# Optimization experiments

Hardware: AMD Instinct MI355X
Metric: run time of the kernel (lower is better)

Reference implementation:

```python
import jax, jax.numpy as jnp
import numpy as np

EMBED_DIM = 1024
NUM_HEADS = 16
HEAD_DIM = EMBED_DIM // NUM_HEADS
B, S = 4, 4096


def maxpool1d_2(x):
    # MaxPooling1D(pool_size=2, strides=2, padding='same'); seq len is even so no padding needed.
    n, l, d = x.shape
    return jnp.max(x.reshape(n, l // 2, 2, d), axis=2)


def setup_inputs() -> dict:
    key = jax.random.key(0)
    ks = jax.random.split(key, 5)
    scale = 1.0 / np.sqrt(EMBED_DIM)
    return {
        "x": jax.random.normal(ks[0], (B, S, EMBED_DIM), dtype=jnp.float32),
        "Wq": jax.random.normal(ks[1], (EMBED_DIM, EMBED_DIM), dtype=jnp.float32) * scale,
        "bq": jnp.zeros((EMBED_DIM,), dtype=jnp.float32),
        "Wk": jax.random.normal(ks[2], (EMBED_DIM, EMBED_DIM), dtype=jnp.float32) * scale,
        "bk": jnp.zeros((EMBED_DIM,), dtype=jnp.float32),
        "Wv": jax.random.normal(ks[3], (EMBED_DIM, EMBED_DIM), dtype=jnp.float32) * scale,
        "bv": jnp.zeros((EMBED_DIM,), dtype=jnp.float32),
        "Wo": jax.random.normal(ks[4], (EMBED_DIM, EMBED_DIM), dtype=jnp.float32) * scale,
        "bo": jnp.zeros((EMBED_DIM,), dtype=jnp.float32),
    }


def _separate_heads_pool(x, batch_size):
    # [B, S, E] -> [B, S, H, hd] -> [B, H, S, hd] -> [B*H, S, hd] -> pooled [B*H, S/2, hd]
    n, s, _ = x.shape
    x = x.reshape(batch_size, s, NUM_HEADS, HEAD_DIM).transpose(0, 2, 1, 3)
    x = x.reshape(batch_size * NUM_HEADS, s, HEAD_DIM)
    return maxpool1d_2(x)


def reference(x, Wq, bq, Wk, bk, Wv, bv, Wo, bo):
    batch_size = x.shape[0]
    q = x @ Wq + bq
    k = x @ Wk + bk
    v = x @ Wv + bv
    q = _separate_heads_pool(q, batch_size)  # [B*H, S/2, hd]
    k = _separate_heads_pool(k, batch_size)
    v = _separate_heads_pool(v, batch_size)
    score = jnp.einsum('nqd,nkd->nqk', q, k) / jnp.sqrt(jnp.float32(HEAD_DIM))
    weights = jax.nn.softmax(score, axis=-1)
    attn = jnp.einsum('nqk,nkd->nqd', weights, v)  # [B*H, S/2, hd]
    attn = maxpool1d_2(attn)  # [B*H, S/4, hd]
    # reshape back: (batch, -1, head_dim*num_heads). NOTE: original reshapes
    # [B*H, S/4, hd] directly to (B, -1, E) without transposing heads back,
    # so we replicate that exact layout.
    attn = attn.reshape(batch_size, -1, HEAD_DIM * NUM_HEADS)  # [B, S/4 (head-major mix), E]
    return attn @ Wo + bo
```

## Files before the change

kernel.cpp:

```cpp
#include <hip/hip_runtime.h>
#include <stdint.h>

typedef __attribute__((ext_vector_type(8))) __bf16 bf16x8;
typedef __attribute__((ext_vector_type(4))) float f32x4;
typedef __attribute__((ext_vector_type(8))) int i32x8;

#define DEV __device__ __forceinline__

DEV unsigned short f2bf(float f) {
  union { float f; uint32_t u; } v; v.f = f;
  return (unsigned short)((v.u + 0x7fffu + ((v.u >> 16) & 1u)) >> 16);
}

DEV uint32_t pk2bf(float lo, float hi) {
  union { float f; uint32_t u; } a, b;
  a.f = lo; b.f = hi;
  return __builtin_amdgcn_perm(b.u + 0x8000u, a.u + 0x8000u, 0x07060302u);
}

DEV void gld16(const void* g, void* l) {
  __builtin_amdgcn_global_load_lds(
      (const __attribute__((address_space(1))) uint32_t*)g,
      (__attribute__((address_space(3))) uint32_t*)l, 16, 0, 0);
}

union Frag8 { i32x8 v; uint4 q[2]; };

__global__ __launch_bounds__(256) void k_cvt_x(const float* __restrict__ x,
                                               uint8_t* __restrict__ x8) {
  size_t t = (size_t)blockIdx.x * 256 + threadIdx.x;
  const float4* xv = (const float4*)x;
  float4 a = xv[t * 2], b = xv[t * 2 + 1];
  int lo = 0, hi = 0;
  lo = __builtin_amdgcn_cvt_pk_fp8_f32(a.x, a.y, lo, false);
  lo = __builtin_amdgcn_cvt_pk_fp8_f32(a.z, a.w, lo, true);
  hi = __builtin_amdgcn_cvt_pk_fp8_f32(b.x, b.y, hi, false);
  hi = __builtin_amdgcn_cvt_pk_fp8_f32(b.z, b.w, hi, true);
  int2 pk; pk.x = lo; pk.y = hi;
  *(int2*)&x8[t * 8] = pk;
}

__global__ void k_cvt_w(const float* __restrict__ W0, const float* __restrict__ W1,
                        const float* __restrict__ W2, const float* __restrict__ W3,
                        uint8_t* __restrict__ W8, unsigned short* __restrict__ WoT) {
  const int z = blockIdx.z;
  const float* W = (z == 0) ? W0 : (z == 1) ? W1 : (z == 2) ? W2 : W3;
  __shared__ float tile[32][33];
  const int n0 = blockIdx.x * 32, k0 = blockIdx.y * 32;
  const int tx = threadIdx.x, ty = threadIdx.y;
  const int tid = ty * 32 + tx;
#pragma unroll
  for (int i = 0; i < 4; i++)
    tile[ty * 4 + i][tx] = W[(size_t)(k0 + ty * 4 + i) * 1024 + n0 + tx];
  __syncthreads();
  if (z < 3) {
    int nn = tid >> 3, kg = tid & 7;
    int w_ = 0;
    w_ = __builtin_amdgcn_cvt_pk_fp8_f32(32.f * tile[kg * 4 + 0][nn],
                                         32.f * tile[kg * 4 + 1][nn], w_, false);
    w_ = __builtin_amdgcn_cvt_pk_fp8_f32(32.f * tile[kg * 4 + 2][nn],
                                         32.f * tile[kg * 4 + 3][nn], w_, true);
    *(uint32_t*)&W8[(size_t)z * 1048576 + (size_t)(n0 + nn) * 1024 + k0 + kg * 4] =
        (uint32_t)w_;
  } else {
#pragma unroll
    for (int i = 0; i < 4; i++)
      WoT[(size_t)(n0 + ty * 4 + i) * 1024 + k0 + tx] = f2bf(tile[tx][ty * 4 + i]);
  }
}

__global__ __launch_bounds__(256) void k_gemm_qkv(
    const uint8_t* __restrict__ A, const uint8_t* __restrict__ W8,
    const float* __restrict__ bq, const float* __restrict__ bk,
    const float* __restrict__ bv,
    unsigned short* __restrict__ Qp, unsigned short* __restrict__ Kp,
    unsigned short* __restrict__ Vt) {
  const int tid = threadIdx.x;
  const int n0 = blockIdx.x * 128, m0 = blockIdx.y * 128;
  const int z = blockIdx.z;
  const uint8_t* Bt = W8 + (size_t)z * 1048576;
  const float* bias = (z == 0) ? bq : (z == 1) ? bk : bv;

  __shared__ __align__(16) uint8_t lA[128 * 128];
  __shared__ __align__(16) uint8_t lB[128 * 128];

  const int lane = tid & 63, w = tid >> 6;
  const int wr = w >> 1, wc = w & 1;
  const int r = lane & 15, qd = lane >> 4;
  const int rl = lane >> 3, sg = lane & 7;

  f32x4 acc[4][4];
#pragma unroll
  for (int i = 0; i < 4; i++)
#pragma unroll
    for (int j = 0; j < 4; j++) acc[i][j] = (f32x4){0.f, 0.f, 0.f, 0.f};

  for (int k0 = 0; k0 < 1024; k0 += 128) {
    __syncthreads();
#pragma unroll
    for (int p = 0; p < 4; p++) {
      int row = (p * 4 + w) * 8 + rl;
      int g = sg ^ (row & 7);
      gld16(&A[(size_t)(m0 + row) * 1024 + k0 + g * 16], &lA[row * 128 + sg * 16]);
      gld16(&Bt[(size_t)(n0 + row) * 1024 + k0 + g * 16], &lB[row * 128 + sg * 16]);
    }
    __syncthreads();
    Frag8 bfr[4];
#pragma unroll
    for (int nt = 0; nt < 4; nt++) {
      int row = wc * 64 + nt * 16 + r;
      int g0 = (2 * qd) ^ (row & 7), g1 = (2 * qd + 1) ^ (row & 7);
      bfr[nt].q[0] = *(const uint4*)&lB[row * 128 + g0 * 16];
      bfr[nt].q[1] = *(const uint4*)&lB[row * 128 + g1 * 16];
    }
#pragma unroll
    for (int mt = 0; mt < 4; mt++) {
      int row = wr * 64 + mt * 16 + r;
      int g0 = (2 * qd) ^ (row & 7), g1 = (2 * qd + 1) ^ (row & 7);
      Frag8 af;
      af.q[0] = *(const uint4*)&lA[row * 128 + g0 * 16];
      af.q[1] = *(const uint4*)&lA[row * 128 + g1 * 16];
#pragma unroll
      for (int nt = 0; nt < 4; nt++)
        acc[mt][nt] = __builtin_amdgcn_mfma_scale_f32_16x16x128_f8f6f4(
            af.v, bfr[nt].v, acc[mt][nt], 0, 0, 0, 0x7f7f7f7f, 0, 0x7f7f7f7f);
    }
  }

  unsigned short* OP = (z == 0) ? Qp : Kp;
#pragma unroll
  for (int nt = 0; nt < 4; nt++) {
    int n = n0 + wc * 64 + nt * 16 + r;
    float bv_ = bias[n];
    int h = n >> 6, d = n & 63;
#pragma unroll
    for (int mt = 0; mt < 4; mt++) {
      int mg = m0 + wr * 64 + mt * 16 + qd * 4;
      int b = mg >> 12, s2 = (mg & 4095) >> 1;
      int bh = b * 16 + h;
      f32x4 a = acc[mt][nt];
      float v0 = fmaxf(a.x, a.y) * 0.03125f + bv_;
      float v1 = fmaxf(a.z, a.w) * 0.03125f + bv_;
      if (z == 2) {
        uint32_t pk = (uint32_t)f2bf(v0) | ((uint32_t)f2bf(v1) << 16);
        *(uint32_t*)&Vt[((size_t)bh * 64 + d) * 2048 + s2] = pk;
      } else {
        size_t base = ((size_t)bh * 2048 + s2) * 64 + d;
        OP[base] = f2bf(v0);
        OP[base + 64] = f2bf(v1);
      }
    }
  }
}

__global__ __launch_bounds__(256) void k_gemm_out(
    const unsigned short* __restrict__ A, const unsigned short* __restrict__ Bt,
    const float* __restrict__ bias, float* __restrict__ fout) {
  const int tid = threadIdx.x;
  const int n0 = blockIdx.x * 128, m0 = blockIdx.y * 128;

  __shared__ __align__(16) unsigned short lA[128 * 64];
  __shared__ __align__(16) unsigned short lB[128 * 64];

  const int lane = tid & 63, w = tid >> 6;
  const int wr = w >> 1, wc = w & 1;
  const int r = lane & 15, qd = lane >> 4;
  const int srow = tid >> 3, sg = tid & 7;

  f32x4 acc[4][4];
#pragma unroll
  for (int i = 0; i < 4; i++)
#pragma unroll
    for (int j = 0; j < 4; j++) acc[i][j] = (f32x4){0.f, 0.f, 0.f, 0.f};

  for (int k0 = 0; k0 < 1024; k0 += 64) {
    __syncthreads();
#pragma unroll
    for (int p = 0; p < 4; p++) {
      int row = p * 32 + srow;
      int gs = sg ^ (row & 7);
      gld16(&A[(size_t)(m0 + row) * 1024 + k0 + gs * 8], &lA[row * 64 + sg * 8]);
      gld16(&Bt[(size_t)(n0 + row) * 1024 + k0 + gs * 8], &lB[row * 64 + sg * 8]);
    }
    __syncthreads();
#pragma unroll
    for (int kf = 0; kf < 2; kf++) {
      bf16x8 af[4], bfr[4];
#pragma unroll
      for (int mt = 0; mt < 4; mt++) {
        int row = wr * 64 + mt * 16 + r;
        int lg = (kf * 4 + qd) ^ (row & 7);
        af[mt] = *(const bf16x8*)&lA[row * 64 + lg * 8];
      }
#pragma unroll
      for (int nt = 0; nt < 4; nt++) {
        int row = wc * 64 + nt * 16 + r;
        int lg = (kf * 4 + qd) ^ (row & 7);
        bfr[nt] = *(const bf16x8*)&lB[row * 64 + lg * 8];
      }
#pragma unroll
      for (int mt = 0; mt < 4; mt++)
#pragma unroll
        for (int nt = 0; nt < 4; nt++)
          acc[mt][nt] = __builtin_amdgcn_mfma_f32_16x16x32_bf16(af[mt], bfr[nt],
                                                               acc[mt][nt], 0, 0, 0);
    }
  }

#pragma unroll
  for (int nt = 0; nt < 4; nt++) {
    int n = n0 + wc * 64 + nt * 16 + r;
    float bv = bias[n];
#pragma unroll
    for (int mt = 0; mt < 4; mt++) {
      int mg = m0 + wr * 64 + mt * 16 + qd * 4;
      f32x4 a = acc[mt][nt];
      fout[(size_t)(mg + 0) * 1024 + n] = a.x + bv;
      fout[(size_t)(mg + 1) * 1024 + n] = a.y + bv;
      fout[(size_t)(mg + 2) * 1024 + n] = a.z + bv;
      fout[(size_t)(mg + 3) * 1024 + n] = a.w + bv;
    }
  }
}

__global__ __launch_bounds__(256) void k_attn(const unsigned short* __restrict__ Qp,
                                              const unsigned short* __restrict__ Kp,
                                              const unsigned short* __restrict__ Vt,
                                              unsigned short* __restrict__ Am) {
  const int tid = threadIdx.x;
  const int qt = blockIdx.x, bh = blockIdx.y;
  const int w = tid >> 6, lane = tid & 63;
  const int r = lane & 15, qd = lane >> 4;
  const int srow = tid >> 3, sg = tid & 7;

  __shared__ __align__(16) unsigned short lK[64 * 64];
  __shared__ __align__(16) unsigned short lV[64 * 64];
  __shared__ __align__(16) unsigned short lP[4][16 * 80];

  const int q0 = qt * 64;
  const int qrow = q0 + w * 16 + r;
  const size_t qbase = ((size_t)bh * 2048 + qrow) * 64;
  const bf16x8 bq0 = *(const bf16x8*)&Qp[qbase + qd * 8];
  const bf16x8 bq1 = *(const bf16x8*)&Qp[qbase + 32 + qd * 8];

  const unsigned short* Kg = Kp + (size_t)bh * 2048 * 64;
  const unsigned short* Vg = Vt + (size_t)bh * 64 * 2048;

  const float K2 = 0.125f * 1.44269504f;

  float lsum = 0.f;
  f32x4 accO[4];
#pragma unroll
  for (int i = 0; i < 4; i++) accO[i] = (f32x4){0.f, 0.f, 0.f, 0.f};

  char* lPw = (char*)&lP[w][0];

  for (int kb = 0; kb < 2048; kb += 64) {
    __syncthreads();
#pragma unroll
    for (int c = 0; c < 2; c++) {
      int row = c * 32 + srow;
      int gs = sg ^ (row & 7);
      gld16(&Kg[(size_t)(kb + row) * 64 + gs * 8], &lK[row * 64 + sg * 8]);
      gld16(&Vg[(size_t)row * 2048 + kb + gs * 8], &lV[row * 64 + sg * 8]);
    }
    __syncthreads();

    f32x4 s[4];
#pragma unroll
    for (int mt = 0; mt < 4; mt++) {
      int row = mt * 16 + r;
      int lg0 = qd ^ (row & 7), lg1 = (4 + qd) ^ (row & 7);
      bf16x8 ak0 = *(const bf16x8*)&lK[row * 64 + lg0 * 8];
      bf16x8 ak1 = *(const bf16x8*)&lK[row * 64 + lg1 * 8];
      s[mt] = (f32x4){0.f, 0.f, 0.f, 0.f};
      s[mt] = __builtin_amdgcn_mfma_f32_16x16x32_bf16(ak0, bq0, s[mt], 0, 0, 0);
      s[mt] = __builtin_amdgcn_mfma_f32_16x16x32_bf16(ak1, bq1, s[mt], 0, 0, 0);
    }

#pragma unroll
    for (int mt = 0; mt < 4; mt++) {
      float p0 = __builtin_amdgcn_exp2f(fmaf(s[mt][0], K2, -0.5f));
      float p1 = __builtin_amdgcn_exp2f(fmaf(s[mt][1], K2, -0.5f));
      float p2 = __builtin_amdgcn_exp2f(fmaf(s[mt][2], K2, -0.5f));
      float p3 = __builtin_amdgcn_exp2f(fmaf(s[mt][3], K2, -0.5f));
      lsum += (p0 + p1) + (p2 + p3);
      uint2 dw; dw.x = pk2bf(p0, p1); dw.y = pk2bf(p2, p3);
      int off = r * 160 + (((2 * mt + (qd >> 1)) ^ (r & 7)) << 4) + ((qd & 1) << 3);
      *(uint2*)(lPw + off) = dw;
    }

    bf16x8 ap0 = *(const bf16x8*)(lPw + r * 160 + ((qd ^ (r & 7)) << 4));
    bf16x8 ap1 = *(const bf16x8*)(lPw + r * 160 + (((4 + qd) ^ (r & 7)) << 4));

#pragma unroll
    for (int nt = 0; nt < 4; nt++) {
      int row = nt * 16 + r;
      int lg0 = qd ^ (row & 7), lg1 = (4 + qd) ^ (row & 7);
      bf16x8 bv0 = *(const bf16x8*)&lV[row * 64 + lg0 * 8];
      bf16x8 bv1 = *(const bf16x8*)&lV[row * 64 + lg1 * 8];
      accO[nt] = __builtin_amdgcn_mfma_f32_16x16x32_bf16(ap0, bv0, accO[nt], 0, 0, 0);
      accO[nt] = __builtin_amdgcn_mfma_f32_16x16x32_bf16(ap1, bv1, accO[nt], 0, 0, 0);
    }
  }

  lsum += __shfl_xor(lsum, 16, 64);
  lsum += __shfl_xor(lsum, 32, 64);
  float linv = 1.f / lsum;
  float inv[4];
#pragma unroll
  for (int g = 0; g < 4; g++) inv[g] = __shfl(linv, qd * 4 + g, 64);

#pragma unroll
  for (int nt = 0; nt < 4; nt++) {
    int d = nt * 16 + r;
    int s4 = (q0 + w * 16 + qd * 4) >> 1;
    float o0 = fmaxf(accO[nt][0] * inv[0], accO[nt][1] * inv[1]);
    float o1 = fmaxf(accO[nt][2] * inv[2], accO[nt][3] * inv[3]);
    size_t base = ((size_t)bh * 1024 + s4) * 64 + d;
    Am[base] = f2bf(o0);
    Am[base + 64] = f2bf(o1);
  }
}

extern "C" void kernel_launch(void* const* d_in, const int* in_sizes, int n_in,
                              void* d_out, int out_size, void* d_ws, size_t ws_size,
                              hipStream_t stream) {
  const float* x  = (const float*)d_in[0];
  const float* Wq = (const float*)d_in[1];
  const float* bq = (const float*)d_in[2];
  const float* Wk = (const float*)d_in[3];
  const float* bk = (const float*)d_in[4];
  const float* Wv = (const float*)d_in[5];
  const float* bv = (const float*)d_in[6];
  const float* Wo = (const float*)d_in[7];
  const float* bo = (const float*)d_in[8];
  float* out = (float*)d_out;

  uint8_t* ws = (uint8_t*)d_ws;
  uint8_t*        x8  = ws;
  uint8_t*        W8  = ws + 16777216;
  unsigned short* WoT = (unsigned short*)(ws + 19922944);
  unsigned short* Qp  = (unsigned short*)(ws + 22020096);
  unsigned short* Kp  = (unsigned short*)(ws + 38797312);
  unsigned short* Vt  = (unsigned short*)(ws + 55574528);
  unsigned short* Am  = (unsigned short*)(ws + 72351744);

  k_cvt_x<<<8192, 256, 0, stream>>>(x, x8);
  k_cvt_w<<<dim3(32, 32, 4), dim3(32, 8), 0, stream>>>(Wq, Wk, Wv, Wo, W8, WoT);
  k_gemm_qkv<<<dim3(8, 128, 3), 256, 0, stream>>>(x8, W8, bq, bk, bv, Qp, Kp, Vt);
  k_attn<<<dim3(32, 64), 256, 0, stream>>>(Qp, Kp, Vt, Am);
  k_gemm_out<<<dim3(8, 32), 256, 0, stream>>>(Am, WoT, bo, out);
}
```

Before: 377.0 us.

## Restructure QKV GEMM: 512 threads, double-buffered A in LDS, B read directly

The QKV fp8 GEMM now runs 8 waves per block in a 2x4 wave grid, with each wave owning a 64x32 output tile. The A tile is double-buffered in LDS so the next k-slice can load while MFMAs run. B fragments are read straight from global memory into registers instead of being staged through LDS, which cuts LDS traffic and one barrier per iteration. The cost is higher global/L2 pressure and exposed latency on the direct B loads.

```diff
diff --git a/kernel.cpp b/kernel.cpp
--- a/kernel.cpp
+++ b/kernel.cpp
@@ -69,7 +69,7 @@
   }
 }
 
-__global__ __launch_bounds__(256) void k_gemm_qkv(
+__global__ __launch_bounds__(512, 4) void k_gemm_qkv(
     const uint8_t* __restrict__ A, const uint8_t* __restrict__ W8,
     const float* __restrict__ bq, const float* __restrict__ bk,
     const float* __restrict__ bv,
@@ -81,47 +81,54 @@
   const uint8_t* Bt = W8 + (size_t)z * 1048576;
   const float* bias = (z == 0) ? bq : (z == 1) ? bk : bv;
 
-  __shared__ __align__(16) uint8_t lA[128 * 128];
-  __shared__ __align__(16) uint8_t lB[128 * 128];
+  __shared__ __align__(16) uint8_t lA[2][128 * 128];
 
   const int lane = tid & 63, w = tid >> 6;
-  const int wr = w >> 1, wc = w & 1;
+  const int wm = w >> 2, wn = w & 3;
   const int r = lane & 15, qd = lane >> 4;
-  const int rl = lane >> 3, sg = lane & 7;
-
-  f32x4 acc[4][4];
+  const int rl = tid >> 3, sg = tid & 7;
+
+  f32x4 acc[4][2];
 #pragma unroll
   for (int i = 0; i < 4; i++)
 #pragma unroll
-    for (int j = 0; j < 4; j++) acc[i][j] = (f32x4){0.f, 0.f, 0.f, 0.f};
-
-  for (int k0 = 0; k0 < 1024; k0 += 128) {
-    __syncthreads();
-#pragma unroll
-    for (int p = 0; p < 4; p++) {
-      int row = (p * 4 + w) * 8 + rl;
+    for (int j = 0; j < 2; j++) acc[i][j] = (f32x4){0.f, 0.f, 0.f, 0.f};
+
+  const uint8_t* Bw = Bt + (size_t)(n0 + wn * 32 + r) * 1024 + qd * 32;
+
+  auto stage = [&](int buf, int k0) {
+#pragma unroll
+    for (int p = 0; p < 2; p++) {
+      int row = p * 64 + rl;
       int g = sg ^ (row & 7);
-      gld16(&A[(size_t)(m0 + row) * 1024 + k0 + g * 16], &lA[row * 128 + sg * 16]);
-      gld16(&Bt[(size_t)(n0 + row) * 1024 + k0 + g * 16], &lB[row * 128 + sg * 16]);
-    }
-    __syncthreads();
-    Frag8 bfr[4];
-#pragma unroll
-    for (int nt = 0; nt < 4; nt++) {
-      int row = wc * 64 + nt * 16 + r;
-      int g0 = (2 * qd) ^ (row & 7), g1 = (2 * qd + 1) ^ (row & 7);
-      bfr[nt].q[0] = *(const uint4*)&lB[row * 128 + g0 * 16];
-      bfr[nt].q[1] = *(const uint4*)&lB[row * 128 + g1 * 16];
-    }
-#pragma unroll
-    for (int mt = 0; mt < 4; mt++) {
-      int row = wr * 64 + mt * 16 + r;
+      gld16(&A[(size_t)(m0 + row) * 1024 + k0 + g * 16],
+            &lA[buf][row * 128 + sg * 16]);
+    }
+  };
+
+  stage(0, 0);
+  for (int kb = 0; kb < 8; kb++) {
+    const int k0 = kb * 128;
+    __syncthreads();
+    if (kb < 7) stage((kb + 1) & 1, k0 + 128);
+
+    Frag8 bfr[2];
+#pragma unroll
+    for (int nt = 0; nt < 2; nt++) {
+      bfr[nt].q[0] = *(const uint4*)(Bw + nt * 16384 + k0);
+      bfr[nt].q[1] = *(const uint4*)(Bw + nt * 16384 + k0 + 16);
+    }
+
+    const uint8_t* lAb = &lA[kb & 1][0];
+#pragma unroll
+    for (int mt = 0; mt < 4; mt++) {
+      int row = wm * 64 + mt * 16 + r;
       int g0 = (2 * qd) ^ (row & 7), g1 = (2 * qd + 1) ^ (row & 7);
       Frag8 af;
-      af.q[0] = *(const uint4*)&lA[row * 128 + g0 * 16];
-      af.q[1] = *(const uint4*)&lA[row * 128 + g1 * 16];
-#pragma unroll
-      for (int nt = 0; nt < 4; nt++)
+      af.q[0] = *(const uint4*)&lAb[row * 128 + g0 * 16];
+      af.q[1] = *(const uint4*)&lAb[row * 128 + g1 * 16];
+#pragma unroll
+      for (int nt = 0; nt < 2; nt++)
         acc[mt][nt] = __builtin_amdgcn_mfma_scale_f32_16x16x128_f8f6f4(
             af.v, bfr[nt].v, acc[mt][nt], 0, 0, 0, 0x7f7f7f7f, 0, 0x7f7f7f7f);
     }
@@ -129,13 +136,13 @@
 
   unsigned short* OP = (z == 0) ? Qp : Kp;
 #pragma unroll
-  for (int nt = 0; nt < 4; nt++) {
-    int n = n0 + wc * 64 + nt * 16 + r;
+  for (int nt = 0; nt < 2; nt++) {
+    int n = n0 + wn * 32 + nt * 16 + r;
     float bv_ = bias[n];
     int h = n >> 6, d = n & 63;
 #pragma unroll
     for (int mt = 0; mt < 4; mt++) {
-      int mg = m0 + wr * 64 + mt * 16 + qd * 4;
+      int mg = m0 + wm * 64 + mt * 16 + qd * 4;
       int b = mg >> 12, s2 = (mg & 4095) >> 1;
       int bh = b * 16 + h;
       f32x4 a = acc[mt][nt];
@@ -348,7 +355,7 @@
 
   k_cvt_x<<<8192, 256, 0, stream>>>(x, x8);
   k_cvt_w<<<dim3(32, 32, 4), dim3(32, 8), 0, stream>>>(Wq, Wk, Wv, Wo, W8, WoT);
-  k_gemm_qkv<<<dim3(8, 128, 3), 256, 0, stream>>>(x8, W8, bq, bk, bv, Qp, Kp, Vt);
+  k_gemm_qkv<<<dim3(8, 128, 3), 512, 0, stream>>>(x8, W8, bq, bk, bv, Qp, Kp, Vt);
   k_attn<<<dim3(32, 64), 256, 0, stream>>>(Qp, Kp, Vt, Am);
   k_gemm_out<<<dim3(8, 32), 256, 0, stream>>>(Am, WoT, bo, out);
 }
```

After: 1.199 ms. 218% more time.
